# Kernel tuning notes

Measured on AMD Instinct MI355X. Metric: run time of the kernel, lower is better.

Reference implementation:

```python
import jax, jax.numpy as jnp
import numpy as np

R = 8192   # rows of the input matrix (attention sequence dim)
F = 4096   # total input feature columns
L = 2048   # number of gathered columns (len(in_keys))


def setup_inputs() -> dict:
    key = jax.random.key(0)
    k1, k2, k3 = jax.random.split(key, 3)
    inputs = jax.random.normal(k1, (R, F), dtype=jnp.float32)
    in_idxs = jax.random.randint(k2, (L,), 0, F)
    weights = jax.random.normal(k3, (L, 3), dtype=jnp.float32)
    return {"inputs": inputs, "in_idxs": in_idxs, "weights": weights}


def reference(inputs, in_idxs, weights):
    # gather: torch.index_select(inputs, 1, in_idxs) -> [R, L]
    sel = jnp.take(inputs, in_idxs, axis=1)
    # QKV projection: [R, L] @ [L, 3] -> [R, 3]; chunk -> q, k, v each [R, 1]
    qkv = sel @ weights
    q, k, v = qkv[:, 0:1], qkv[:, 1:2], qkv[:, 2:3]
    d_k = q.shape[-1]  # = 1
    # scaled dot-product attention over the row dim: logits [R, R]
    logits = (q @ k.T) / jnp.sqrt(jnp.float32(d_k))
    attn = jax.nn.softmax(logits, axis=-1)
    values = attn @ v  # [R, 1]
    # out = activation(values[-1:, ]) -> [1, 1]
    return jax.nn.sigmoid(values[-1:, :])
```

## Files before the change

kernel.cpp:

```cpp
#include <hip/hip_runtime.h>
#include <math.h>

#define RR 8192
#define FF 4096
#define LL 2048
#define NBLK 1024
#define TPB 512

#define WS_W1  0
#define WS_W2  FF
#define WS_Q   (2 * FF)
#define WS_P   (2 * FF + 16)

__global__ __launch_bounds__(1024) void prep(const float* __restrict__ in,
                                             const int* __restrict__ idx,
                                             const float* __restrict__ wts,
                                             float* __restrict__ ws) {
    __shared__ float wsh[FF];
    __shared__ float qred[16];

    const int t = threadIdx.x, lane = t & 63, wv = t >> 6;
    const int b = blockIdx.x;

    for (int i = t; i < FF; i += 1024) wsh[i] = 0.f;
    __syncthreads();

    if (b == 0) {
        const float* lastrow = in + (size_t)(RR - 1) * FF;
        float qp = 0.f;
#pragma unroll
        for (int l = t; l < LL; l += 1024) {
            const int c = idx[l];
            qp += lastrow[c] * wts[3 * l + 0];
            atomicAdd(&wsh[c], wts[3 * l + 1]);
        }
        for (int o = 32; o > 0; o >>= 1) qp += __shfl_down(qp, o);
        if (lane == 0) qred[wv] = qp;
        __syncthreads();
        if (t < FF / 4)
            *(float4*)(ws + WS_W1 + t * 4) = *(const float4*)&wsh[t * 4];
        if (t == 0) {
            float q = 0.f;
#pragma unroll
            for (int i = 0; i < 16; ++i) q += qred[i];
            ws[WS_Q] = q;
        }
    } else {
#pragma unroll
        for (int l = t; l < LL; l += 1024) {
            atomicAdd(&wsh[idx[l]], wts[3 * l + 2]);
        }
        __syncthreads();
        if (t < FF / 4)
            *(float4*)(ws + WS_W2 + t * 4) = *(const float4*)&wsh[t * 4];
    }
}

__global__ __launch_bounds__(TPB) void gemv_kv(const float* __restrict__ in,
                                               const float* __restrict__ ws,
                                               float* __restrict__ partials) {
    __shared__ float w1s[FF];
    __shared__ float w2s[FF];
    __shared__ float kv[8][2];

    const int t = threadIdx.x, lane = t & 63, wv = t >> 6;

    for (int i = t; i < FF / 4; i += TPB) {
        *(float4*)&w1s[i * 4] = *(const float4*)(ws + WS_W1 + i * 4);
        *(float4*)&w2s[i * 4] = *(const float4*)(ws + WS_W2 + i * 4);
    }
    __syncthreads();

    const int row = blockIdx.x * 8 + wv;
    const float* __restrict__ x = in + (size_t)row * FF;

    float k = 0.f, v = 0.f;
#pragma unroll
    for (int i = 0; i < FF; i += 256) {
        const int c = i + lane * 4;
        const float4 xv = *(const float4*)(x + c);
        const float4 a1 = *(const float4*)&w1s[c];
        const float4 a2 = *(const float4*)&w2s[c];
        k += xv.x * a1.x + xv.y * a1.y + xv.z * a1.z + xv.w * a1.w;
        v += xv.x * a2.x + xv.y * a2.y + xv.z * a2.z + xv.w * a2.w;
    }
    for (int o = 32; o > 0; o >>= 1) { k += __shfl_down(k, o); v += __shfl_down(v, o); }
    if (lane == 0) { kv[wv][0] = k; kv[wv][1] = v; }
    __syncthreads();

    if (t == 0) {
        const float q = ws[WS_Q];
        float m = -INFINITY;
#pragma unroll
        for (int r = 0; r < 8; ++r) m = fmaxf(m, q * kv[r][0]);
        float se = 0.f, sv = 0.f;
#pragma unroll
        for (int r = 0; r < 8; ++r) {
            const float e = expf(q * kv[r][0] - m);
            se += e;
            sv += e * kv[r][1];
        }
        partials[blockIdx.x * 3 + 0] = m;
        partials[blockIdx.x * 3 + 1] = se;
        partials[blockIdx.x * 3 + 2] = sv;
    }
}

__global__ __launch_bounds__(TPB) void combine(const float* __restrict__ partials,
                                               float* __restrict__ out) {
    const int t = threadIdx.x, lane = t & 63, wv = t >> 6;
    float lm[2], lse[2], lsv[2];
    float m = -INFINITY;
#pragma unroll
    for (int i = 0; i < 2; ++i) {
        const int b = t + i * TPB;
        lm[i]  = partials[b * 3 + 0];
        lse[i] = partials[b * 3 + 1];
        lsv[i] = partials[b * 3 + 2];
        m = fmaxf(m, lm[i]);
    }

    __shared__ float red[8], red2[8], red3[8], bc[1];
    for (int o = 32; o > 0; o >>= 1) m = fmaxf(m, __shfl_down(m, o));
    if (lane == 0) red[wv] = m;
    __syncthreads();
    if (t == 0) {
        float x = red[0];
#pragma unroll
        for (int i = 1; i < 8; ++i) x = fmaxf(x, red[i]);
        bc[0] = x;
    }
    __syncthreads();
    const float gm = bc[0];

    float se = 0.f, sv = 0.f;
#pragma unroll
    for (int i = 0; i < 2; ++i) {
        const float s = expf(lm[i] - gm);
        se += lse[i] * s;
        sv += lsv[i] * s;
    }
    for (int o = 32; o > 0; o >>= 1) { se += __shfl_down(se, o); sv += __shfl_down(sv, o); }
    if (lane == 0) { red2[wv] = se; red3[wv] = sv; }
    __syncthreads();
    if (t == 0) {
        float S = 0.f, V = 0.f;
#pragma unroll
        for (int i = 0; i < 8; ++i) { S += red2[i]; V += red3[i]; }
        out[0] = 1.0f / (1.0f + expf(-(V / S)));
    }
}

extern "C" void kernel_launch(void* const* d_in, const int* in_sizes, int n_in,
                              void* d_out, int out_size, void* d_ws, size_t ws_size,
                              hipStream_t stream) {
    const float* inputs = (const float*)d_in[0];
    const int*   idx    = (const int*)d_in[1];
    const float* wts    = (const float*)d_in[2];
    float* out = (float*)d_out;
    float* ws  = (float*)d_ws;

    prep<<<2, 1024, 0, stream>>>(inputs, idx, wts, ws);
    gemv_kv<<<NBLK, TPB, 0, stream>>>(inputs, ws, ws + WS_P);
    combine<<<1, TPB, 0, stream>>>(ws + WS_P, out);
}
```

Before: 34.95 us.

## Stream input rows into LDS with async global_load_lds double buffering

Each wave now streams its input row through a per-wave double-buffered LDS staging area using the global_load_lds builtin. The first two chunks are issued before the weight vectors are copied to shared memory, and waits use explicit vmcnt counters. The intent is to overlap the row stream with the weight staging and the compute, and to keep more loads in flight than plain register loads allow. The cost is extra LDS (a further 32KB per block), which lowers occupancy. It also depends on the vmcnt accounting being right; the q load and the weight loads share the counter, and the LDS reads carry no explicit lgkm wait.

```diff
diff --git a/kernel.cpp b/kernel.cpp
--- a/kernel.cpp
+++ b/kernel.cpp
@@ -11,6 +11,13 @@
 #define WS_W2  FF
 #define WS_Q   (2 * FF)
 #define WS_P   (2 * FF + 16)
+
+typedef const __attribute__((address_space(1))) unsigned int gu32;
+typedef __attribute__((address_space(3))) unsigned int lu32;
+
+__device__ __forceinline__ void ld_lds16(const float* g, float* l) {
+    __builtin_amdgcn_global_load_lds((gu32*)g, (lu32*)l, 16, 0, 0);
+}
 
 __global__ __launch_bounds__(1024) void prep(const float* __restrict__ in,
                                              const int* __restrict__ idx,
@@ -61,9 +68,23 @@
                                                float* __restrict__ partials) {
     __shared__ float w1s[FF];
     __shared__ float w2s[FF];
+    __shared__ float xbuf[8][2][512];
     __shared__ float kv[8][2];
 
     const int t = threadIdx.x, lane = t & 63, wv = t >> 6;
+    const int row = blockIdx.x * 8 + wv;
+    const float* __restrict__ xrow = in + (size_t)row * FF;
+
+#define ISSUE(ch, buf) do {                                      \
+        const float* gsrc = xrow + (ch) * 512 + lane * 4;        \
+        ld_lds16(gsrc,       &xbuf[wv][buf][0]);                 \
+        ld_lds16(gsrc + 256, &xbuf[wv][buf][256]);               \
+    } while (0)
+
+    ISSUE(0, 0);
+    ISSUE(1, 1);
+
+    const float q = ws[WS_Q];
 
     for (int i = t; i < FF / 4; i += TPB) {
         *(float4*)&w1s[i * 4] = *(const float4*)(ws + WS_W1 + i * 4);
@@ -71,25 +92,35 @@
     }
     __syncthreads();
 
-    const int row = blockIdx.x * 8 + wv;
-    const float* __restrict__ x = in + (size_t)row * FF;
-
     float k = 0.f, v = 0.f;
 #pragma unroll
-    for (int i = 0; i < FF; i += 256) {
-        const int c = i + lane * 4;
-        const float4 xv = *(const float4*)(x + c);
-        const float4 a1 = *(const float4*)&w1s[c];
-        const float4 a2 = *(const float4*)&w2s[c];
-        k += xv.x * a1.x + xv.y * a1.y + xv.z * a1.z + xv.w * a1.w;
-        v += xv.x * a2.x + xv.y * a2.y + xv.z * a2.z + xv.w * a2.w;
+    for (int ch = 0; ch < 8; ++ch) {
+        const int buf = ch & 1;
+        if (ch < 7) asm volatile("s_waitcnt vmcnt(2)" ::: "memory");
+        else        asm volatile("s_waitcnt vmcnt(0)" ::: "memory");
+
+        const float4 r0 = *(const float4*)&xbuf[wv][buf][lane * 4];
+        const float4 r1 = *(const float4*)&xbuf[wv][buf][256 + lane * 4];
+
+        const int c0 = ch * 512 + lane * 4;
+        const float4 a10 = *(const float4*)&w1s[c0];
+        const float4 a20 = *(const float4*)&w2s[c0];
+        k += r0.x * a10.x + r0.y * a10.y + r0.z * a10.z + r0.w * a10.w;
+        v += r0.x * a20.x + r0.y * a20.y + r0.z * a20.z + r0.w * a20.w;
+        const float4 a11 = *(const float4*)&w1s[c0 + 256];
+        const float4 a21 = *(const float4*)&w2s[c0 + 256];
+        k += r1.x * a11.x + r1.y * a11.y + r1.z * a11.z + r1.w * a11.w;
+        v += r1.x * a21.x + r1.y * a21.y + r1.z * a21.z + r1.w * a21.w;
+
+        if (ch < 6) ISSUE(ch + 2, buf);
     }
+#undef ISSUE
+
     for (int o = 32; o > 0; o >>= 1) { k += __shfl_down(k, o); v += __shfl_down(v, o); }
     if (lane == 0) { kv[wv][0] = k; kv[wv][1] = v; }
     __syncthreads();
 
     if (t == 0) {
-        const float q = ws[WS_Q];
         float m = -INFINITY;
 #pragma unroll
         for (int r = 0; r < 8; ++r) m = fmaxf(m, q * kv[r][0]);
```

After: 35.40 us. No clear change (+1.3%).
